# Optimization experiments

Measured on AMD Instinct MI355X. Metric: run time of the kernel, lower is better.

## Reference

```python
import jax, jax.numpy as jnp
import numpy as np


def setup_inputs() -> dict:
    key = jax.random.key(0)
    ks = jax.random.split(key, 12)
    C, H, L, P = 256, 8, 4, 4
    Lq, Lx = 2048, 300
    iss = jnp.array([[64, 64], [32, 32], [16, 16], [8, 8]], dtype=jnp.int32)
    Len_in = int(np.sum(np.array(iss)[:, 0] * np.array(iss)[:, 1]))  # 5440
    lsi = jnp.array([0, 4096, 5120, 5376], dtype=jnp.int32)
    return {
        "query": jax.random.normal(ks[0], (1, Lq, C), jnp.float32),
        "reference_points": jax.random.uniform(ks[1], (1, Lq, L, 2), jnp.float32),
        "input_flatten": jax.random.normal(ks[2], (1, Len_in, C), jnp.float32),
        "input_spatial_shapes": iss,
        "add_keys": jax.random.normal(ks[3], (1, Lx, C), jnp.float32),
        "input_level_start_index": lsi,
        "W_off": jax.random.normal(ks[4], (H * L * P * 2, C), jnp.float32) * 0.01,
        "b_off": jax.random.normal(ks[5], (H * L * P * 2,), jnp.float32),
        "W_attn": jax.random.normal(ks[6], (H * (L + 1), C, C), jnp.float32) * 0.05,
        "W_v": jax.random.normal(ks[7], (H * 2, C, C), jnp.float32) * 0.05,
        "b_v": jax.random.normal(ks[8], (H * 2, C), jnp.float32) * 0.01,
        "W_mix": jax.random.normal(ks[9], (C, H + 1), jnp.float32) * 0.5,
    }


def reference(query, reference_points, input_flatten, input_spatial_shapes,
              add_keys, input_level_start_index, W_off, b_off, W_attn, W_v, b_v, W_mix):
    N, Lq, C = query.shape
    L = input_spatial_shapes.shape[0]
    H = W_v.shape[0] // 2
    P = W_off.shape[0] // (H * L * 2)

    # sampling locations: ref (x,y in [0,1]) + offsets / (W,H)
    off = (query @ W_off.T + b_off).reshape(N, Lq, H, L, P, 2)
    wh = input_spatial_shapes[:, ::-1].astype(query.dtype)  # (L,2) = (W,H)
    loc = reference_points[:, :, None, :, None, :] + off / wh[None, None, None, :, None, :]

    # get_keys: truncating index computation + gather (faithful to original)
    loc = jnp.clip(loc, 0.0, 0.999)
    iss_f = input_spatial_shapes.astype(loc.dtype)[None, None, None, :, None, :]
    idx = (loc * iss_f).astype(jnp.int32)  # (N,Lq,H,L,P,2): (int(x*H_l), int(y*W_l))
    lin = (idx[..., 0]
           + idx[..., 1] * input_spatial_shapes[:, 0].astype(jnp.int32)[None, None, None, :, None]
           + input_level_start_index.astype(jnp.int32)[None, None, None, :, None])
    keys = input_flatten[0][lin[0]]                # (Lq,H,L,P,C)
    keys = jnp.transpose(keys, (1, 2, 3, 0, 4))    # (H,L,P,Lq,C)

    head_w = jax.nn.softmax(W_mix.T, axis=0)       # (H+1,C)
    qf = query[0]                                  # (Lq,C)
    ak = add_keys[0]                               # (Lx,C)

    # per-head, per-level similarity (replicates original overlapping index h*L+lvl)
    Ws = W_attn[jnp.arange(H)[:, None] * L + jnp.arange(L)[None, :]]  # (H,L,C,C)
    T = jnp.einsum('hlce,hlpqe->hlcpq', Ws, keys)  # (H,L,C,P,Lq)
    # faithful reshape quirk: (C, P*Lq) viewed as (P, Lq, C)
    T = T.reshape(H, L, P, Lq, C)
    attn_s = jnp.einsum('hlpqc,qc->hlpq', T, qf).reshape(H, L * P, Lq)

    Wadd = W_attn[jnp.arange(H) * L + L]           # (H,C,C)
    attn_a = jnp.einsum('xe,hce,qc->hxq', ak, Wadd, qf)  # (H,Lx,Lq)

    attn = jax.nn.softmax(jnp.concatenate([attn_s, attn_a], axis=1), axis=1)
    attn_s_sm, attn_a_sm = attn[:, :L * P], attn[:, L * P:]

    Wv0, bv0 = W_v[0::2], b_v[0::2]
    Wv1, bv1 = W_v[1::2], b_v[1::2]
    vals = (jnp.einsum('hlpqe,hce->hlpqc', keys, Wv0)
            + bv0[:, None, None, None, :]).reshape(H, L * P, Lq, C)
    v2 = jnp.einsum('xe,hce->hxc', ak, Wv1) + bv1[:, None, :]  # (H,Lx,C)

    out_h = (jnp.einsum('hkq,hkqc->hqc', attn_s_sm, vals)
             + jnp.einsum('hxq,hxc->hqc', attn_a_sm, v2))      # (H,Lq,C)
    result = qf * head_w[-1][None, :] + jnp.einsum('hqc,hc->qc', out_h, head_w[:-1])
    return result[None]
```

## Files before the change

### kernel.cpp

```cpp
#include <hip/hip_runtime.h>
#include <stdint.h>

#define NJ 316

typedef __attribute__((ext_vector_type(8))) short short8;
typedef __attribute__((ext_vector_type(4))) float f32x4;
union U4S8 { uint4 u; short8 s; };

__device__ __forceinline__ unsigned short f2bf(float x) {
    unsigned int u = __float_as_uint(x);
    u += 0x7fff + ((u >> 16) & 1);
    return (unsigned short)(u >> 16);
}
__device__ __forceinline__ float bf2f(unsigned short h) {
    return __uint_as_float(((unsigned int)h) << 16);
}

struct Seg {
    const unsigned short *Ah, *Al, *Bh, *Bl;
    int K, lda, ldb;
    long sA, sB;
    int nprod;
};

template<bool ACCUM, bool OUTF32, int NSEG>
__device__ __forceinline__ void gemm_core(
    const Seg& s0, const Seg& s1,
    float* __restrict__ Cf, unsigned short* __restrict__ Ch,
    unsigned short* __restrict__ Cl,
    int M, int N, int ldc, long sC, int nb, int mb, int z, char* smem)
{
    unsigned short* As0 = (unsigned short*)smem;
    unsigned short* Bs0 = (unsigned short*)(smem + 10240);
    const int t = threadIdx.x;
    const int lane = t & 63;
    const int wave = t >> 6;
    const int wm = (wave & 1) * 32, wn = (wave >> 1) * 64;

    f32x4 acc[2][4];
    #pragma unroll
    for (int i = 0; i < 2; ++i)
        #pragma unroll
        for (int j = 0; j < 4; ++j) acc[i][j] = (f32x4){0.f, 0.f, 0.f, 0.f};

    const int arow = t >> 2, akoff = (t & 3) * 8;
    const int frow = lane & 15, fk = (lane >> 4) * 8;

    #pragma unroll
    for (int seg = 0; seg < NSEG; ++seg) {
        const Seg S = seg ? s1 : s0;
        const int np = S.nprod;
        const unsigned short* Azh = S.Ah + (size_t)z * S.sA;
        const unsigned short* Azl = (np >= 2) ? S.Al + (size_t)z * S.sA : nullptr;
        const unsigned short* Bzh = S.Bh + (size_t)z * S.sB;
        const unsigned short* Bzl = (np >= 3) ? S.Bl + (size_t)z * S.sB : nullptr;
        for (int kb = 0; kb < S.K; kb += 32) {
            __syncthreads();
            {
                int gm = mb + arow;
                uint4 vh = {0, 0, 0, 0}, vl = {0, 0, 0, 0};
                if (gm < M) {
                    size_t o = (size_t)gm * S.lda + kb + akoff;
                    vh = *(const uint4*)(Azh + o);
                    if (np >= 2) vl = *(const uint4*)(Azl + o);
                }
                *(uint4*)&As0[arow * 40 + akoff] = vh;
                if (np >= 2) *(uint4*)&As0[2560 + arow * 40 + akoff] = vl;
                #pragma unroll
                for (int i = 0; i < 2; ++i) {
                    int f = i * 256 + t;
                    int brow = f >> 2, bkoff = (f & 3) * 8;
                    int gn = nb + brow;
                    uint4 wh = {0, 0, 0, 0}, wl = {0, 0, 0, 0};
                    if (gn < N) {
                        size_t o = (size_t)gn * S.ldb + kb + bkoff;
                        wh = *(const uint4*)(Bzh + o);
                        if (np >= 3) wl = *(const uint4*)(Bzl + o);
                    }
                    *(uint4*)&Bs0[brow * 40 + bkoff] = wh;
                    if (np >= 3) *(uint4*)&Bs0[5120 + brow * 40 + bkoff] = wl;
                }
            }
            __syncthreads();
            short8 a[2][2], b[4][2];
            #pragma unroll
            for (int i = 0; i < 2; ++i) {
                int r = wm + i * 16 + frow;
                a[i][0] = *(const short8*)&As0[r * 40 + fk];
                if (np >= 2) a[i][1] = *(const short8*)&As0[2560 + r * 40 + fk];
            }
            #pragma unroll
            for (int j = 0; j < 4; ++j) {
                int r = wn + j * 16 + frow;
                b[j][0] = *(const short8*)&Bs0[r * 40 + fk];
                if (np >= 3) b[j][1] = *(const short8*)&Bs0[5120 + r * 40 + fk];
            }
            #pragma unroll
            for (int i = 0; i < 2; ++i)
                #pragma unroll
                for (int j = 0; j < 4; ++j) {
                    acc[i][j] = __builtin_amdgcn_mfma_f32_16x16x32_bf16(
                        a[i][0], b[j][0], acc[i][j], 0, 0, 0);
                    if (np >= 2)
                        acc[i][j] = __builtin_amdgcn_mfma_f32_16x16x32_bf16(
                            a[i][1], b[j][0], acc[i][j], 0, 0, 0);
                    if (np >= 3)
                        acc[i][j] = __builtin_amdgcn_mfma_f32_16x16x32_bf16(
                            a[i][0], b[j][1], acc[i][j], 0, 0, 0);
                }
        }
    }
    #pragma unroll
    for (int i = 0; i < 2; ++i)
        #pragma unroll
        for (int r = 0; r < 4; ++r) {
            int gm = mb + wm + i * 16 + (lane >> 4) * 4 + r;
            if (gm >= M) continue;
            #pragma unroll
            for (int j = 0; j < 4; ++j) {
                int gn = nb + wn + j * 16 + (lane & 15);
                if (gn >= N) continue;
                size_t idx = (size_t)z * sC + (size_t)gm * ldc + gn;
                float v = acc[i][j][r];
                if (OUTF32) {
                    float prev = ACCUM ? Cf[idx] : 0.f;
                    Cf[idx] = prev + v;
                } else {
                    unsigned short h = f2bf(v);
                    Ch[idx] = h;
                    Cl[idx] = f2bf(v - bf2f(h));
                }
            }
        }
}

template<bool ACCUM, bool OUTF32, int NSEG>
__global__ __launch_bounds__(256) void mfma_gemm(
    Seg s0, Seg s1,
    float* __restrict__ Cf, unsigned short* __restrict__ Ch,
    unsigned short* __restrict__ Cl,
    int M, int N, int ldc, long sC)
{
    __shared__ __align__(16) char smem[30720];
    gemm_core<ACCUM, OUTF32, NSEG>(s0, s1, Cf, Ch, Cl, M, N, ldc, sC,
                                   blockIdx.x * 128, blockIdx.y * 64,
                                   blockIdx.z, smem);
}

__global__ __launch_bounds__(256) void mfma_gemm_dual(
    Seg a, int Ma, int Na, int ldca, long sCa,
    unsigned short* __restrict__ Cha, unsigned short* __restrict__ Cla,
    Seg b, int Mb, int Nb, int ldcb, long sCb,
    unsigned short* __restrict__ Chb, unsigned short* __restrict__ Clb,
    int ax)
{
    __shared__ __align__(16) char smem[30720];
    Seg dummy = a;
    if ((int)blockIdx.x < ax) {
        if ((int)blockIdx.y * 64 >= Ma) return;
        gemm_core<false, false, 1>(a, dummy, nullptr, Cha, Cla,
                                   Ma, Na, ldca, sCa,
                                   blockIdx.x * 128, blockIdx.y * 64,
                                   blockIdx.z, smem);
    } else {
        if ((int)blockIdx.y * 64 >= Mb) return;
        gemm_core<false, false, 1>(b, dummy, nullptr, Chb, Clb,
                                   Mb, Nb, ldcb, sCb,
                                   (blockIdx.x - ax) * 128, blockIdx.y * 64,
                                   blockIdx.z, smem);
    }
}

__global__ __launch_bounds__(256) void cvt_lin_kernel(
    const float* __restrict__ q,  unsigned short* __restrict__ qh,  unsigned short* __restrict__ ql,
    const float* __restrict__ ak, unsigned short* __restrict__ akh, unsigned short* __restrict__ akl,
    const float* __restrict__ wv, unsigned short* __restrict__ wvh, unsigned short* __restrict__ wvl,
    const float* __restrict__ inflat, unsigned int* __restrict__ inflatP,
    const float* __restrict__ Wattn, unsigned short* __restrict__ wah, unsigned short* __restrict__ wal,
    unsigned short* __restrict__ v2th, unsigned short* __restrict__ v2tl,
    const float* __restrict__ refp, const int* __restrict__ iss,
    const int* __restrict__ lsi, const float* __restrict__ Woff,
    const float* __restrict__ boff, int* __restrict__ lin)
{
    __shared__ float qf8[8][256];
    __shared__ float wtile[256][17];
    __shared__ double offl[8][256];
    const int t = threadIdx.x;

    if (blockIdx.x < 3491) {
        int i = blockIdx.x * 256 + t;
        if (i < 760576) {
            const float* s; unsigned short *dh, *dl; int off; bool pack = false;
            unsigned int* dp = nullptr;
            if (i < 131072)      { s = q;  dh = qh;  dl = ql;  off = i; }
            else if (i < 150272) { s = ak; dh = akh; dl = akl; off = i - 131072; }
            else if (i < 412416) { s = wv; dh = wvh; dl = wvl; off = i - 150272; }
            else { s = inflat; dp = inflatP; off = i - 412416; pack = true; dh = dl = nullptr; }
            float4 v = ((const float4*)s)[off];
            float x[4] = {v.x, v.y, v.z, v.w};
            unsigned short h[4], l[4];
            #pragma unroll
            for (int j = 0; j < 4; ++j) {
                h[j] = f2bf(x[j]);
                l[j] = f2bf(x[j] - bf2f(h[j]));
            }
            if (pack) {
                ((uint4*)dp)[off] = make_uint4(
                    (unsigned)h[0] | ((unsigned)l[0] << 16),
                    (unsigned)h[1] | ((unsigned)l[1] << 16),
                    (unsigned)h[2] | ((unsigned)l[2] << 16),
                    (unsigned)h[3] | ((unsigned)l[3] << 16));
            } else {
                ((uint2*)dh)[off] = make_uint2((unsigned)h[0] | ((unsigned)h[1] << 16),
                                               (unsigned)h[2] | ((unsigned)h[3] << 16));
                ((uint2*)dl)[off] = make_uint2((unsigned)l[0] | ((unsigned)l[1] << 16),
                                               (unsigned)l[2] | ((unsigned)l[3] << 16));
            }
        } else if (i < 891648) {
            int off = i - 760576;
            int base = off * 4;
            int z = base >> 16, r = base & 65535;
            float4 v = *(const float4*)&Wattn[(size_t)(4 * z + 4) * 65536 + r];
            float x[4] = {v.x, v.y, v.z, v.w};
            unsigned short h[4], l[4];
            #pragma unroll
            for (int j = 0; j < 4; ++j) {
                h[j] = f2bf(x[j]);
                l[j] = f2bf(x[j] - bf2f(h[j]));
            }
            ((uint2*)wah)[off] = make_uint2((unsigned)h[0] | ((unsigned)h[1] << 16),
                                            (unsigned)h[2] | ((unsigned)h[3] << 16));
            ((uint2*)wal)[off] = make_uint2((unsigned)l[0] | ((unsigned)l[1] << 16),
                                            (unsigned)l[2] | ((unsigned)l[3] << 16));
        } else {
            int j = i - 891648;
            size_t base = (size_t)j * 320;
            uint2 zz = make_uint2(0u, 0u);
            #pragma unroll
            for (int d = 0; d < 4; ++d) {
                ((uint2*)(v2th + base))[d] = zz;
                ((uint2*)(v2tl + base))[d] = zz;
            }
            ((uint2*)(v2th + base + 316))[0] = zz;
            ((uint2*)(v2tl + base + 316))[0] = zz;
        }
        return;
    }

    const int qbase = (blockIdx.x - 3491) * 8;
    #pragma unroll
    for (int i = 0; i < 8; ++i) qf8[i][t] = q[(qbase + i) * 256 + t];
    double acc[8];
    #pragma unroll
    for (int r = 0; r < 8; ++r) acc[r] = 0.0;
    for (int cb = 0; cb < 256; cb += 16) {
        __syncthreads();
        #pragma unroll
        for (int i = 0; i < 16; ++i) {
            int f = i * 256 + t;
            int o = f >> 4, jj = f & 15;
            wtile[o][jj] = Woff[o * 256 + cb + jj];
        }
        __syncthreads();
        #pragma unroll
        for (int jj = 0; jj < 16; ++jj) {
            double wvv = (double)wtile[t][jj];
            #pragma unroll
            for (int r = 0; r < 8; ++r)
                acc[r] += (double)qf8[r][cb + jj] * wvv;
        }
    }
    double bo = (double)boff[t];
    __syncthreads();
    #pragma unroll
    for (int r = 0; r < 8; ++r) offl[r][t] = acc[r] + bo;
    __syncthreads();
    #pragma unroll
    for (int rep = 0; rep < 4; ++rep) {
        int idx = rep * 256 + t;
        int r = idx >> 7;
        int s = idx & 127;
        int l = (s >> 2) & 3;
        int qq = qbase + r;
        double offx = offl[r][2 * s];
        double offy = offl[r][2 * s + 1];
        int w0 = iss[l * 2 + 0];
        int w1 = iss[l * 2 + 1];
        double locx = (double)refp[qq * 8 + l * 2 + 0] + offx / (double)w1;
        double locy = (double)refp[qq * 8 + l * 2 + 1] + offy / (double)w0;
        locx = fmin(fmax(locx, 0.0), 0.999);
        locy = fmin(fmax(locy, 0.0), 0.999);
        int ix = (int)(locx * (double)w0);
        int iy = (int)(locy * (double)w1);
        lin[qq * 128 + s] = ix + iy * w0 + lsi[l];
    }
}

__global__ __launch_bounds__(256, 2) void gattn_attnA(
    const unsigned short* __restrict__ qh, const unsigned short* __restrict__ ql,
    const unsigned int* __restrict__ inflatP, const float* __restrict__ Wattn,
    const int* __restrict__ lin, float* __restrict__ attn, Seg aA)
{
    __shared__ __align__(16) char smem[69632];
    const int t = threadIdx.x;

    if ((int)blockIdx.x >= 1024) {
        int idx = blockIdx.x - 1024;
        int z = idx & 7, my = (idx >> 3) & 31, nx = idx >> 8;
        gemm_core<false, true, 1>(aA, aA, attn + 16, nullptr, nullptr,
                                  2048, 300, NJ, 2048L * NJ,
                                  nx * 128, my * 64, z, smem);
        return;
    }

    int* linrow = (int*)smem;
    float (*Glds)[268] = (float(*)[268])(smem + 1024);
    const int lane = t & 63, w = t >> 6;
    const int b = blockIdx.x;
    const int qb = b & 7, p = (b >> 3) & 3, l = (b >> 5) & 3, h = b >> 7;
    linrow[t] = lin[(256 * qb + t) * 128 + h * 16 + l * 4 + p];
    __syncthreads();

    const int l15 = lane & 15, g = lane >> 4;
    const int q2l = qb + 8 * p + 32 * l15;
    const int ebase = 64 * w + l15;

    f32x4 acc[4][4];
    #pragma unroll
    for (int i = 0; i < 4; ++i)
        #pragma unroll
        for (int eg = 0; eg < 4; ++eg) acc[i][eg] = (f32x4){0.f, 0.f, 0.f, 0.f};

    for (int kb = 0; kb < 256; kb += 32) {
        U4S8 ah[4], al[4];
        #pragma unroll
        for (int i = 0; i < 4; ++i) {
            size_t off = (size_t)(q2l + 512 * i) * 256 + kb + 8 * g;
            ah[i].u = *(const uint4*)(qh + off);
            al[i].u = *(const uint4*)(ql + off);
        }
        int rowoff[8];
        #pragma unroll
        for (int m = 0; m < 8; ++m) rowoff[m] = linrow[kb + 8 * g + m] * 256;
        unsigned int uv[4][8];
        #pragma unroll
        for (int eg = 0; eg < 4; ++eg)
            #pragma unroll
            for (int m = 0; m < 8; ++m)
                uv[eg][m] = inflatP[rowoff[m] + ebase + 16 * eg];

        #pragma unroll
        for (int eg = 0; eg < 4; ++eg) {
            U4S8 bh, bl;
            unsigned int hh[4], ll[4];
            #pragma unroll
            for (int d = 0; d < 4; ++d) {
                hh[d] = __builtin_amdgcn_perm(uv[eg][2 * d + 1], uv[eg][2 * d],
                                              0x05040100u);
                ll[d] = __builtin_amdgcn_perm(uv[eg][2 * d + 1], uv[eg][2 * d],
                                              0x07060302u);
            }
            bh.u = make_uint4(hh[0], hh[1], hh[2], hh[3]);
            bl.u = make_uint4(ll[0], ll[1], ll[2], ll[3]);
            #pragma unroll
            for (int i = 0; i < 4; ++i) {
                acc[i][eg] = __builtin_amdgcn_mfma_f32_16x16x32_bf16(
                    ah[i].s, bh.s, acc[i][eg], 0, 0, 0);
                acc[i][eg] = __builtin_amdgcn_mfma_f32_16x16x32_bf16(
                    ah[i].s, bl.s, acc[i][eg], 0, 0, 0);
                acc[i][eg] = __builtin_amdgcn_mfma_f32_16x16x32_bf16(
                    al[i].s, bh.s, acc[i][eg], 0, 0, 0);
            }
        }
    }

    #pragma unroll
    for (int i = 0; i < 4; ++i)
        #pragma unroll
        for (int eg = 0; eg < 4; ++eg)
            #pragma unroll
            for (int r = 0; r < 4; ++r)
                Glds[16 * i + 4 * g + r][64 * w + 16 * eg + l15] = acc[i][eg][r];
    __syncthreads();

    const int tx = t & 15, ty = t >> 4;
    const float* Wsbase = Wattn + (size_t)(h * 4 + l) * 65536;
    float gv[4][16];
    #pragma unroll
    for (int r = 0; r < 4; ++r)
        #pragma unroll
        for (int i2 = 0; i2 < 4; ++i2) {
            float4 gd = *(const float4*)&Glds[ty * 4 + r][tx * 4 + 64 * i2];
            gv[r][i2 * 4 + 0] = gd.x;
            gv[r][i2 * 4 + 1] = gd.y;
            gv[r][i2 * 4 + 2] = gd.z;
            gv[r][i2 * 4 + 3] = gd.w;
        }
    #pragma unroll
    for (int r = 0; r < 4; ++r) {
        int hi = ty * 4 + r;
        int q2 = qb + 8 * p + 32 * hi;
        #pragma unroll
        for (int p2 = 0; p2 < 4; ++p2) {
            const float* wr = Wsbase + (size_t)(hi + 64 * p2) * 256;
            float partial = 0.f;
            #pragma unroll
            for (int i2 = 0; i2 < 4; ++i2) {
                float4 wv = *(const float4*)&wr[tx * 4 + 64 * i2];
                partial += wv.x * gv[r][i2 * 4 + 0] + wv.y * gv[r][i2 * 4 + 1]
                         + wv.z * gv[r][i2 * 4 + 2] + wv.w * gv[r][i2 * 4 + 3];
            }
            partial += __shfl_xor(partial, 1);
            partial += __shfl_xor(partial, 2);
            partial += __shfl_xor(partial, 4);
            partial += __shfl_xor(partial, 8);
            if (tx == 0)
                attn[((size_t)h * 2048 + q2) * NJ + (l * 4 + p2)] = partial;
        }
    }
}

__global__ __launch_bounds__(256) void softmax_ka_kernel(
    const float* __restrict__ attn, const unsigned int* __restrict__ inflatP,
    const int* __restrict__ lin, float* __restrict__ s0,
    unsigned short* __restrict__ awh,
    unsigned short* __restrict__ KAh, unsigned short* __restrict__ KAl)
{
    __shared__ float red[8];
    __shared__ float w16[16];
    __shared__ int lls[16];
    const int t = threadIdx.x;
    const int lane = t & 63, w = t >> 6;
    const int rid = blockIdx.x;
    const int h = rid >> 11, q = rid & 2047;
    const float* row = attn + (size_t)rid * NJ;

    float v0 = row[t];
    float v1 = (t < 60) ? row[256 + t] : -1e30f;
    float m = fmaxf(v0, v1);
    #pragma unroll
    for (int d = 1; d < 64; d <<= 1) m = fmaxf(m, __shfl_xor(m, d));
    if (lane == 0) red[w] = m;
    __syncthreads();
    m = fmaxf(fmaxf(red[0], red[1]), fmaxf(red[2], red[3]));

    float e0 = expf(v0 - m);
    float e1 = (t < 60) ? expf(v1 - m) : 0.f;
    float s = e0 + e1;
    #pragma unroll
    for (int d = 1; d < 64; d <<= 1) s += __shfl_xor(s, d);
    if (lane == 0) red[4 + w] = s;
    __syncthreads();
    s = (red[4] + red[5]) + (red[6] + red[7]);
    const float inv = 1.f / s;

    float sf = (t < 16) ? e0 : 0.f;
    #pragma unroll
    for (int d = 1; d < 64; d <<= 1) sf += __shfl_xor(sf, d);
    if (lane == 0) red[w] = sf;

    float a0 = e0 * inv;
    float a1 = (t < 60) ? e1 * inv : 0.f;
    awh[(size_t)rid * 320 + t] = f2bf(a0);
    if (t < 64)
        awh[(size_t)rid * 320 + 256 + t] = f2bf(a1);
    if (t < 16) {
        w16[t] = a0;
        lls[t] = lin[q * 128 + h * 16 + t];
    }
    __syncthreads();
    if (t == 0)
        s0[rid] = ((red[0] + red[1]) + (red[2] + red[3])) * inv;

    float acc = 0.f;
    #pragma unroll
    for (int k = 0; k < 16; ++k) {
        unsigned int u = inflatP[lls[k] * 256 + t];
        acc += w16[k] * (bf2f((unsigned short)(u & 0xffff)) +
                         bf2f((unsigned short)(u >> 16)));
    }
    unsigned short hh = f2bf(acc);
    KAh[(size_t)rid * 256 + t] = hh;
    KAl[(size_t)rid * 256 + t] = f2bf(acc - bf2f(hh));
}

__global__ __launch_bounds__(256) void final_kernel(
    const float* __restrict__ qf, const float* __restrict__ OH,
    const float* __restrict__ s0, const float* __restrict__ bv,
    const float* __restrict__ Wmix, float* __restrict__ out)
{
    const int q = blockIdx.x, c = threadIdx.x;
    float wj[9], m = -1e30f;
    #pragma unroll
    for (int j = 0; j < 9; ++j) { wj[j] = Wmix[c * 9 + j]; m = fmaxf(m, wj[j]); }
    float s = 0.f;
    #pragma unroll
    for (int j = 0; j < 9; ++j) { wj[j] = expf(wj[j] - m); s += wj[j]; }
    float inv = 1.f / s;
    float acc = qf[q * 256 + c] * wj[8] * inv;
    #pragma unroll
    for (int h = 0; h < 8; ++h) {
        float s0v = s0[h * 2048 + q];
        float oh = OH[((size_t)h * 2048 + q) * 256 + c]
                 + s0v * bv[(2 * h) * 256 + c]
                 + (1.f - s0v) * bv[(2 * h + 1) * 256 + c];
        acc += oh * wj[h] * inv;
    }
    out[q * 256 + c] = acc;
}

extern "C" void kernel_launch(void* const* d_in, const int* in_sizes, int n_in,
                              void* d_out, int out_size, void* d_ws, size_t ws_size,
                              hipStream_t stream) {
    const float* query = (const float*)d_in[0];
    const float* refp  = (const float*)d_in[1];
    const float* inflat= (const float*)d_in[2];
    const int*   iss   = (const int*)d_in[3];
    const float* ak    = (const float*)d_in[4];
    const int*   lsi   = (const int*)d_in[5];
    const float* Woff  = (const float*)d_in[6];
    const float* boff  = (const float*)d_in[7];
    const float* Wattn = (const float*)d_in[8];
    const float* Wv    = (const float*)d_in[9];
    const float* bv    = (const float*)d_in[10];
    const float* Wmix  = (const float*)d_in[11];
    float* out = (float*)d_out;

    typedef unsigned short us;
    char* ws = (char*)d_ws;
    int* lin    = (int*)ws;   ws += (size_t)262144 * 4;
    float* attn = (float*)ws; ws += (size_t)8 * 2048 * NJ * 4;
    float* s0   = (float*)ws; ws += (size_t)8 * 2048 * 4;
    unsigned int* inflatP = (unsigned int*)ws; ws += (size_t)1392640 * 4;
    us* qh  = (us*)ws; ws += (size_t)524288 * 2;
    us* ql  = (us*)ws; ws += (size_t)524288 * 2;
    us* akh = (us*)ws; ws += (size_t)320 * 256 * 2;
    us* akl = (us*)ws; ws += (size_t)320 * 256 * 2;
    us* Waddh = (us*)ws; ws += (size_t)524288 * 2;
    us* Waddl = (us*)ws; ws += (size_t)524288 * 2;
    us* Wvh = (us*)ws; ws += (size_t)1048576 * 2;
    us* Wvl = (us*)ws; ws += (size_t)1048576 * 2;
    us* Bhh = (us*)ws; ws += (size_t)8 * 320 * 256 * 2;
    us* Bhl = (us*)ws; ws += (size_t)8 * 320 * 256 * 2;
    us* V2Th= (us*)ws; ws += (size_t)8 * 256 * 320 * 2;
    us* V2Tl= (us*)ws; ws += (size_t)8 * 256 * 320 * 2;
    us* awh = (us*)ws; ws += (size_t)8 * 2048 * 320 * 2;
    us* KAh = (us*)ws; ws += (size_t)8 * 2048 * 256 * 2;
    us* KAl = (us*)ws; ws += (size_t)8 * 2048 * 256 * 2;
    float* OH = (float*)ws;   ws += (size_t)8 * 2048 * 256 * 4;

    cvt_lin_kernel<<<3747, 256, 0, stream>>>(
        query, qh, ql, ak, akh, akl, Wv, Wvh, Wvl,
        inflat, inflatP, Wattn, Waddh, Waddl, V2Th, V2Tl,
        refp, iss, lsi, Woff, boff, lin);

    Seg sz = {nullptr, nullptr, nullptr, nullptr, 0, 0, 0, 0L, 0L, 0};

    {
        Seg a = {akh, akl, Waddh, Waddl, 256, 256, 256, 0L, 65536L, 3};
        Seg b = {Wvh + 65536, Wvl + 65536, akh, nullptr, 256, 256, 256,
                 131072L, 0L, 2};
        mfma_gemm_dual<<<dim3(5, 5, 8), 256, 0, stream>>>(
            a, 300, 256, 256, 320L * 256, Bhh, Bhl,
            b, 256, 300, 320, 256L * 320, V2Th + 16, V2Tl + 16, 2);
    }

    {
        Seg aA = {qh, ql, Bhh, Bhl, 256, 256, 256, 0L, 320L * 256, 3};
        gattn_attnA<<<1792, 256, 0, stream>>>(qh, ql, inflatP, Wattn, lin,
                                              attn, aA);
    }

    softmax_ka_kernel<<<16384, 256, 0, stream>>>(attn, inflatP, lin, s0,
                                                 awh, KAh, KAl);

    {
        Seg a = {KAh, KAl, Wvh, nullptr, 256, 256, 256, 2048L * 256,
                 2L * 65536, 2};
        Seg b = {awh, nullptr, V2Th, nullptr, 320, 320, 320, 2048L * 320,
                 256L * 320, 1};
        mfma_gemm<false, true, 2><<<dim3(2, 32, 8), 256, 0, stream>>>(
            a, b, OH, nullptr, nullptr, 2048, 256, 256, 2048L * 256);
    }

    final_kernel<<<2048, 256, 0, stream>>>(query, OH, s0, bv, Wmix, out);
}
```

Baseline: 310.1 us.

## Move sampling-index computation from conversion kernel into dual GEMM kernel

The offset projection and sampling-index (lin) computation is taken out of the conversion kernel and placed in extra blocks of the dual small-GEMM launch. Those blocks now run alongside the Bh and V2T GEMM tiles instead of at the tail of the elementwise conversion pass. The Woff tile staged in shared memory is widened from 16 to 32 columns, which halves the number of sync rounds. In exchange the fused kernel requests about 57KB of shared memory per block, which may reduce occupancy for the GEMM blocks.

Result: faster. 273.1 us (-11.9%).

```diff
diff --git a/kernel.cpp b/kernel.cpp
--- a/kernel.cpp
+++ b/kernel.cpp
@@ -14,6 +14,72 @@
 }
 __device__ __forceinline__ float bf2f(unsigned short h) {
     return __uint_as_float(((unsigned int)h) << 16);
+}
+
+__global__ __launch_bounds__(256) void cvt_all_kernel(
+    const float* __restrict__ q,  unsigned short* __restrict__ qh,  unsigned short* __restrict__ ql,
+    const float* __restrict__ ak, unsigned short* __restrict__ akh, unsigned short* __restrict__ akl,
+    const float* __restrict__ wv, unsigned short* __restrict__ wvh, unsigned short* __restrict__ wvl,
+    const float* __restrict__ inflat, unsigned int* __restrict__ inflatP,
+    const float* __restrict__ Wattn, unsigned short* __restrict__ wah, unsigned short* __restrict__ wal,
+    unsigned short* __restrict__ v2th, unsigned short* __restrict__ v2tl)
+{
+    int i = blockIdx.x * 256 + threadIdx.x;
+    if (i < 760576) {
+        const float* s; unsigned short *dh, *dl; int off; bool pack = false;
+        unsigned int* dp = nullptr;
+        if (i < 131072)      { s = q;  dh = qh;  dl = ql;  off = i; }
+        else if (i < 150272) { s = ak; dh = akh; dl = akl; off = i - 131072; }
+        else if (i < 412416) { s = wv; dh = wvh; dl = wvl; off = i - 150272; }
+        else { s = inflat; dp = inflatP; off = i - 412416; pack = true; dh = dl = nullptr; }
+        float4 v = ((const float4*)s)[off];
+        float x[4] = {v.x, v.y, v.z, v.w};
+        unsigned short h[4], l[4];
+        #pragma unroll
+        for (int j = 0; j < 4; ++j) {
+            h[j] = f2bf(x[j]);
+            l[j] = f2bf(x[j] - bf2f(h[j]));
+        }
+        if (pack) {
+            ((uint4*)dp)[off] = make_uint4(
+                (unsigned)h[0] | ((unsigned)l[0] << 16),
+                (unsigned)h[1] | ((unsigned)l[1] << 16),
+                (unsigned)h[2] | ((unsigned)l[2] << 16),
+                (unsigned)h[3] | ((unsigned)l[3] << 16));
+        } else {
+            ((uint2*)dh)[off] = make_uint2((unsigned)h[0] | ((unsigned)h[1] << 16),
+                                           (unsigned)h[2] | ((unsigned)h[3] << 16));
+            ((uint2*)dl)[off] = make_uint2((unsigned)l[0] | ((unsigned)l[1] << 16),
+                                           (unsigned)l[2] | ((unsigned)l[3] << 16));
+        }
+    } else if (i < 891648) {
+        int off = i - 760576;
+        int base = off * 4;
+        int z = base >> 16, r = base & 65535;
+        float4 v = *(const float4*)&Wattn[(size_t)(4 * z + 4) * 65536 + r];
+        float x[4] = {v.x, v.y, v.z, v.w};
+        unsigned short h[4], l[4];
+        #pragma unroll
+        for (int j = 0; j < 4; ++j) {
+            h[j] = f2bf(x[j]);
+            l[j] = f2bf(x[j] - bf2f(h[j]));
+        }
+        ((uint2*)wah)[off] = make_uint2((unsigned)h[0] | ((unsigned)h[1] << 16),
+                                        (unsigned)h[2] | ((unsigned)h[3] << 16));
+        ((uint2*)wal)[off] = make_uint2((unsigned)l[0] | ((unsigned)l[1] << 16),
+                                        (unsigned)l[2] | ((unsigned)l[3] << 16));
+    } else {
+        int j = i - 891648;
+        size_t base = (size_t)j * 320;
+        uint2 zz = make_uint2(0u, 0u);
+        #pragma unroll
+        for (int d = 0; d < 4; ++d) {
+            ((uint2*)(v2th + base))[d] = zz;
+            ((uint2*)(v2tl + base))[d] = zz;
+        }
+        ((uint2*)(v2th + base + 316))[0] = zz;
+        ((uint2*)(v2tl + base + 316))[0] = zz;
+    }
 }
 
 struct Seg {
@@ -147,123 +213,55 @@
                                    blockIdx.z, smem);
 }
 
-__global__ __launch_bounds__(256) void mfma_gemm_dual(
-    Seg a, int Ma, int Na, int ldca, long sCa,
-    unsigned short* __restrict__ Cha, unsigned short* __restrict__ Cla,
-    Seg b, int Mb, int Nb, int ldcb, long sCb,
-    unsigned short* __restrict__ Chb, unsigned short* __restrict__ Clb,
-    int ax)
-{
-    __shared__ __align__(16) char smem[30720];
-    Seg dummy = a;
-    if ((int)blockIdx.x < ax) {
-        if ((int)blockIdx.y * 64 >= Ma) return;
-        gemm_core<false, false, 1>(a, dummy, nullptr, Cha, Cla,
-                                   Ma, Na, ldca, sCa,
-                                   blockIdx.x * 128, blockIdx.y * 64,
-                                   blockIdx.z, smem);
-    } else {
-        if ((int)blockIdx.y * 64 >= Mb) return;
-        gemm_core<false, false, 1>(b, dummy, nullptr, Chb, Clb,
-                                   Mb, Nb, ldcb, sCb,
-                                   (blockIdx.x - ax) * 128, blockIdx.y * 64,
-                                   blockIdx.z, smem);
-    }
-}
-
-__global__ __launch_bounds__(256) void cvt_lin_kernel(
-    const float* __restrict__ q,  unsigned short* __restrict__ qh,  unsigned short* __restrict__ ql,
-    const float* __restrict__ ak, unsigned short* __restrict__ akh, unsigned short* __restrict__ akl,
-    const float* __restrict__ wv, unsigned short* __restrict__ wvh, unsigned short* __restrict__ wvl,
-    const float* __restrict__ inflat, unsigned int* __restrict__ inflatP,
-    const float* __restrict__ Wattn, unsigned short* __restrict__ wah, unsigned short* __restrict__ wal,
-    unsigned short* __restrict__ v2th, unsigned short* __restrict__ v2tl,
-    const float* __restrict__ refp, const int* __restrict__ iss,
-    const int* __restrict__ lsi, const float* __restrict__ Woff,
-    const float* __restrict__ boff, int* __restrict__ lin)
-{
-    __shared__ float qf8[8][256];
-    __shared__ float wtile[256][17];
-    __shared__ double offl[8][256];
+__global__ __launch_bounds__(256) void dual_lin_kernel(
+    Seg a, Seg b,
+    unsigned short* __restrict__ Bhh, unsigned short* __restrict__ Bhl,
+    unsigned short* __restrict__ V2Th, unsigned short* __restrict__ V2Tl,
+    const float* __restrict__ q, const float* __restrict__ refp,
+    const int* __restrict__ iss, const int* __restrict__ lsi,
+    const float* __restrict__ Woff, const float* __restrict__ boff,
+    int* __restrict__ lin)
+{
+    __shared__ __align__(16) char smem[58368];
+    const int bx = blockIdx.x;
+    if (bx < 2) {
+        gemm_core<false, false, 1>(a, a, nullptr, Bhh, Bhl,
+                                   300, 256, 256, 320L * 256,
+                                   bx * 128, blockIdx.y * 64, blockIdx.z, smem);
+        return;
+    }
+    if (bx < 5) {
+        if ((int)blockIdx.y * 64 >= 256) return;
+        gemm_core<false, false, 1>(b, b, nullptr, V2Th, V2Tl,
+                                   256, 300, 320, 256L * 320,
+                                   (bx - 2) * 128, blockIdx.y * 64, blockIdx.z,
+                                   smem);
+        return;
+    }
+    const int idx = (bx - 5) * 40 + blockIdx.y * 8 + blockIdx.z;
+    if (idx >= 256) return;
+
+    float (*qf8)[256]  = (float(*)[256])smem;
+    float (*wtile)[33] = (float(*)[33])(smem + 8192);
+    double (*offl)[256]= (double(*)[256])(smem + 41984);
     const int t = threadIdx.x;
-
-    if (blockIdx.x < 3491) {
-        int i = blockIdx.x * 256 + t;
-        if (i < 760576) {
-            const float* s; unsigned short *dh, *dl; int off; bool pack = false;
-            unsigned int* dp = nullptr;
-            if (i < 131072)      { s = q;  dh = qh;  dl = ql;  off = i; }
-            else if (i < 150272) { s = ak; dh = akh; dl = akl; off = i - 131072; }
-            else if (i < 412416) { s = wv; dh = wvh; dl = wvl; off = i - 150272; }
-            else { s = inflat; dp = inflatP; off = i - 412416; pack = true; dh = dl = nullptr; }
-            float4 v = ((const float4*)s)[off];
-            float x[4] = {v.x, v.y, v.z, v.w};
-            unsigned short h[4], l[4];
-            #pragma unroll
-            for (int j = 0; j < 4; ++j) {
-                h[j] = f2bf(x[j]);
-                l[j] = f2bf(x[j] - bf2f(h[j]));
-            }
-            if (pack) {
-                ((uint4*)dp)[off] = make_uint4(
-                    (unsigned)h[0] | ((unsigned)l[0] << 16),
-                    (unsigned)h[1] | ((unsigned)l[1] << 16),
-                    (unsigned)h[2] | ((unsigned)l[2] << 16),
-                    (unsigned)h[3] | ((unsigned)l[3] << 16));
-            } else {
-                ((uint2*)dh)[off] = make_uint2((unsigned)h[0] | ((unsigned)h[1] << 16),
-                                               (unsigned)h[2] | ((unsigned)h[3] << 16));
-                ((uint2*)dl)[off] = make_uint2((unsigned)l[0] | ((unsigned)l[1] << 16),
-                                               (unsigned)l[2] | ((unsigned)l[3] << 16));
-            }
-        } else if (i < 891648) {
-            int off = i - 760576;
-            int base = off * 4;
-            int z = base >> 16, r = base & 65535;
-            float4 v = *(const float4*)&Wattn[(size_t)(4 * z + 4) * 65536 + r];
-            float x[4] = {v.x, v.y, v.z, v.w};
-            unsigned short h[4], l[4];
-            #pragma unroll
-            for (int j = 0; j < 4; ++j) {
-                h[j] = f2bf(x[j]);
-                l[j] = f2bf(x[j] - bf2f(h[j]));
-            }
-            ((uint2*)wah)[off] = make_uint2((unsigned)h[0] | ((unsigned)h[1] << 16),
-                                            (unsigned)h[2] | ((unsigned)h[3] << 16));
-            ((uint2*)wal)[off] = make_uint2((unsigned)l[0] | ((unsigned)l[1] << 16),
-                                            (unsigned)l[2] | ((unsigned)l[3] << 16));
-        } else {
-            int j = i - 891648;
-            size_t base = (size_t)j * 320;
-            uint2 zz = make_uint2(0u, 0u);
-            #pragma unroll
-            for (int d = 0; d < 4; ++d) {
-                ((uint2*)(v2th + base))[d] = zz;
-                ((uint2*)(v2tl + base))[d] = zz;
-            }
-            ((uint2*)(v2th + base + 316))[0] = zz;
-            ((uint2*)(v2tl + base + 316))[0] = zz;
-        }
-        return;
-    }
-
-    const int qbase = (blockIdx.x - 3491) * 8;
+    const int qbase = idx * 8;
     #pragma unroll
     for (int i = 0; i < 8; ++i) qf8[i][t] = q[(qbase + i) * 256 + t];
     double acc[8];
     #pragma unroll
     for (int r = 0; r < 8; ++r) acc[r] = 0.0;
-    for (int cb = 0; cb < 256; cb += 16) {
+    for (int cb = 0; cb < 256; cb += 32) {
         __syncthreads();
         #pragma unroll
-        for (int i = 0; i < 16; ++i) {
+        for (int i = 0; i < 32; ++i) {
             int f = i * 256 + t;
-            int o = f >> 4, jj = f & 15;
+            int o = f >> 5, jj = f & 31;
             wtile[o][jj] = Woff[o * 256 + cb + jj];
         }
         __syncthreads();
         #pragma unroll
-        for (int jj = 0; jj < 16; ++jj) {
+        for (int jj = 0; jj < 32; ++jj) {
             double wvv = (double)wtile[t][jj];
             #pragma unroll
             for (int r = 0; r < 8; ++r)
@@ -277,9 +275,9 @@
     __syncthreads();
     #pragma unroll
     for (int rep = 0; rep < 4; ++rep) {
-        int idx = rep * 256 + t;
-        int r = idx >> 7;
-        int s = idx & 127;
+        int id2 = rep * 256 + t;
+        int r = id2 >> 7;
+        int s = id2 & 127;
         int l = (s >> 2) & 3;
         int qq = qbase + r;
         double offx = offl[r][2 * s];
@@ -549,10 +547,9 @@
     us* KAl = (us*)ws; ws += (size_t)8 * 2048 * 256 * 2;
     float* OH = (float*)ws;   ws += (size_t)8 * 2048 * 256 * 4;
 
-    cvt_lin_kernel<<<3747, 256, 0, stream>>>(
+    cvt_all_kernel<<<3491, 256, 0, stream>>>(
         query, qh, ql, ak, akh, akl, Wv, Wvh, Wvl,
-        inflat, inflatP, Wattn, Waddh, Waddl, V2Th, V2Tl,
-        refp, iss, lsi, Woff, boff, lin);
+        inflat, inflatP, Wattn, Waddh, Waddl, V2Th, V2Tl);
 
     Seg sz = {nullptr, nullptr, nullptr, nullptr, 0, 0, 0, 0L, 0L, 0};
 
@@ -560,9 +557,9 @@
         Seg a = {akh, akl, Waddh, Waddl, 256, 256, 256, 0L, 65536L, 3};
         Seg b = {Wvh + 65536, Wvl + 65536, akh, nullptr, 256, 256, 256,
                  131072L, 0L, 2};
-        mfma_gemm_dual<<<dim3(5, 5, 8), 256, 0, stream>>>(
-            a, 300, 256, 256, 320L * 256, Bhh, Bhl,
-            b, 256, 300, 320, 256L * 320, V2Th + 16, V2Tl + 16, 2);
+        dual_lin_kernel<<<dim3(12, 5, 8), 256, 0, stream>>>(
+            a, b, Bhh, Bhl, V2Th + 16, V2Tl + 16,
+            query, refp, iss, lsi, Woff, boff, lin);
     }
 
     {
```
